# Performance work log

Measured on AMD Instinct MI355X. Metric: run time of the kernel, lower is better.

## Reference

```python
import jax, jax.numpy as jnp
import numpy as np

B, N, S, K, NDIM, HID = 2, 8192, 1024, 32, 3, 256


def _sincos_embed(pos, dim):
    # pos: (..., ndim) continuous coordinates -> (..., dim) sincos embedding
    ndim = pos.shape[-1]
    emb_dim_per_dim = dim // ndim
    half = emb_dim_per_dim // 2
    freq = jnp.exp(jnp.arange(half, dtype=pos.dtype) * (-np.log(10000.0) / (half - 1)))
    embs = []
    for i in range(ndim):
        e = pos[..., i:i + 1] * freq  # (..., half)
        embs.append(jnp.concatenate([jnp.sin(e), jnp.cos(e)], axis=-1))
    x = jnp.concatenate(embs, axis=-1)  # (..., ndim*2*half)
    pad = dim - x.shape[-1]
    if pad > 0:
        x = jnp.pad(x, [(0, 0)] * (x.ndim - 1) + [(0, pad)])
    return x


def setup_inputs() -> dict:
    key = jax.random.key(0)
    ks = jax.random.split(key, 8)
    input_pos = jax.random.normal(ks[0], (B, N, NDIM), dtype=jnp.float32)
    supernode_idxs = jax.random.randint(ks[1], (S,), 0, N)
    # lecun_normal-style init (stddev = 1/sqrt(fan_in)), zero bias (torch/flax Dense default bias=0)
    w_in = jax.random.normal(ks[2], (NDIM, HID), dtype=jnp.float32) / np.sqrt(NDIM)
    b_in = jnp.zeros((HID,), jnp.float32)
    w1 = jax.random.normal(ks[3], (HID, HID), dtype=jnp.float32) / np.sqrt(HID)
    b1 = jnp.zeros((HID,), jnp.float32)
    w2 = jax.random.normal(ks[4], (HID, HID), dtype=jnp.float32) / np.sqrt(HID)
    b2 = jnp.zeros((HID,), jnp.float32)
    return {"input_pos": input_pos, "supernode_idxs": supernode_idxs,
            "w_in": w_in, "b_in": b_in, "w1": w1, "b1": b1, "w2": w2, "b2": b2}


def reference(input_pos, supernode_idxs, w_in, b_in, w1, b1, w2, b2):
    def knn(x):  # x: (N, ndim)
        # Euclidean distance from each supernode to every point: (S, N).
        # Same values as rows of the full NxN cdist the original materializes.
        d = jnp.sqrt(jnp.sum((x[supernode_idxs][:, None, :] - x[None, :, :]) ** 2, axis=-1))
        nbr = jnp.argsort(d, axis=1)[:, :K]  # (S, K)
        return x[nbr]  # (S, K, ndim)

    coords = jax.vmap(knn)(input_pos)  # (B, S, K, ndim)
    proj = coords @ w_in + b_in                         # (B, S, K, HID)
    pe = _sincos_embed(coords, HID)                     # (B, S, K, HID)
    h = proj + pe
    h = jax.nn.gelu(h @ w1 + b1) @ w2 + b2              # message MLP
    return jnp.mean(h, axis=-2)                         # (B, S, HID)
```

## Files before the change

### kernel.cpp

```cpp
#include <hip/hip_runtime.h>
#include <hip/hip_bf16.h>
#include <math.h>

#define BB   2
#define NN   8192
#define SS   1024
#define KK   32
#define HID  256
#define NTH  256
#define PPT  64
#define SENT 0xFFFFFFFFFFFFFFFFULL
#define LDB  264
#define WFE  65536

typedef unsigned long long u64;
typedef unsigned int       u32;
typedef short bf16x8 __attribute__((ext_vector_type(8)));
typedef float f32x4  __attribute__((ext_vector_type(4)));

#define CSW(SI) { const u64 mn = x < (SI) ? x : (SI); const u64 mx = x < (SI) ? (SI) : x; (SI) = mn; x = mx; }
#define INS(KV) { u64 x = (KV); CSW(s0) CSW(s1) CSW(s2) CSW(s3) }

__device__ __forceinline__ float tanh_fast(float y) {
    const float e = __expf(2.0f * y);
    const float r = __builtin_amdgcn_rcpf(e + 1.0f);
    return fmaf(-2.0f, r, 1.0f);
}

__device__ __forceinline__ short bf_bits(float f) {
    const __hip_bfloat16 h = __float2bfloat16(f);
    short s;
    __builtin_memcpy(&s, &h, 2);
    return s;
}

__device__ __forceinline__ int mbcnt64(u64 m) {
    return (int)__builtin_amdgcn_mbcnt_hi((u32)(m >> 32),
           __builtin_amdgcn_mbcnt_lo((u32)m, 0u));
}

__global__ void prep_w(const float* __restrict__ w1, const float* __restrict__ w2,
                       __hip_bfloat16* __restrict__ wf) {
    const int idx = blockIdx.x * 256 + threadIdx.x;
    const int j   = idx & 7;
    const int l   = (idx >> 3) & 63;
    const int ntg = (idx >> 9) & 15;
    const int ks  = (idx >> 13) & 7;
    const int mat = idx >> 16;
    const int k = ks * 32 + (l >> 4) * 8 + j;
    const int n = ntg * 16 + (l & 15);
    const float v = (mat ? w2 : w1)[k * HID + n];
    const __hip_bfloat16 hi = __float2bfloat16(v);
    const float res = v - __bfloat162float(hi);
    const size_t s0 = (size_t)mat * 131072 + ((size_t)((ks*16 + ntg)*2) * 64 + l) * 8 + j;
    wf[s0]       = hi;
    wf[s0 + 512] = __float2bfloat16(res);
}

__global__ __launch_bounds__(NTH, 4)
void snp_kernel(const float* __restrict__ pos,
                const int*   __restrict__ snidx,
                const float* __restrict__ w_in,
                const float* __restrict__ b_in,
                const float* __restrict__ b1,
                const float* __restrict__ b2,
                const __hip_bfloat16* __restrict__ wf,
                float*       __restrict__ out)
{
    const int tk0  = blockIdx.x * 2;
    const int b    = tk0 / SS;
    const int s0i  = tk0 - b * SS;
    const int t    = threadIdx.x;
    const int lane = t & 63;
    const int wv   = t >> 6;
    const int tok  = t >> 7;
    const int pl   = t & 127;

    __shared__ __align__(16) short h0b[2 * KK][LDB];
    __shared__ u64   wl[4 * KK];
    __shared__ int   nbr[2 * KK];
    __shared__ __align__(16) float nbc[2 * 4 * KK];

    const float* posb = pos + (size_t)b * (NN * 3);
    const int  spA = snidx[s0i], spB = snidx[s0i + 1];
    const int  sp  = tok ? spB : spA;
    const float sx = posb[sp*3 + 0];
    const float sy = posb[sp*3 + 1];
    const float sz = posb[sp*3 + 2];

    u64 s0=SENT,s1=SENT,s2=SENT,s3=SENT;
#pragma unroll 4
    for (int c = 0; c < PPT; ++c) {
        const int i = c * 128 + pl;
        const float dx = __fsub_rn(sx, posb[i*3 + 0]);
        const float dy = __fsub_rn(sy, posb[i*3 + 1]);
        const float dz = __fsub_rn(sz, posb[i*3 + 2]);
        const float sq = __fadd_rn(__fadd_rn(__fmul_rn(dx,dx), __fmul_rn(dy,dy)),
                                   __fmul_rn(dz,dz));
        const u64 kv = ((u64)__float_as_uint(__fsqrt_rn(sq)) << 13) | (u32)i;
        INS(kv);
    }

    {
        u64 L = 0;
        for (int bit = 43; bit >= 13; --bit) {
            const u64 cand = L | (1ull << bit);
            const int cnt = __popcll(__ballot(s0 < cand)) + __popcll(__ballot(s1 < cand))
                          + __popcll(__ballot(s2 < cand)) + __popcll(__ballot(s3 < cand));
            if (cnt < 32) L = cand;
        }
        u64 TH = L + (1ull << 13);
        {
            const int cnt = __popcll(__ballot(s0 < TH)) + __popcll(__ballot(s1 < TH))
                          + __popcll(__ballot(s2 < TH)) + __popcll(__ballot(s3 < TH));
            if (cnt != 32) {
                for (int bit = 12; bit >= 0; --bit) {
                    const u64 cand = L | (1ull << bit);
                    const int c2 = __popcll(__ballot(s0 < cand)) + __popcll(__ballot(s1 < cand))
                                 + __popcll(__ballot(s2 < cand)) + __popcll(__ballot(s3 < cand));
                    if (c2 < 32) L = cand;
                }
                TH = L + 1;
            }
        }
        const bool b0 = s0 < TH, b1 = s1 < TH, b2 = s2 < TH, b3 = s3 < TH;
        const int csel = (int)b0 + (int)b1 + (int)b2 + (int)b3;

        if (__ballot(csel == 4) != 0ull) {
            int nv = 4;
#pragma unroll 1
            for (int it = 0; it < KK; ++it) {
                u64 m = s0;
#pragma unroll
                for (int off = 32; off > 0; off >>= 1) {
                    const u64 o = __shfl_xor(m, off, 64);
                    m = o < m ? o : m;
                }
                if (lane == 0) wl[wv*KK + it] = m;
                if (s0 == m) {
                    s0=s1; s1=s2; s2=s3; s3=SENT;
                    if (--nv == 0) {
                        const u64 last = m;
                        s0=s1=s2=s3=SENT;
#pragma unroll 4
                        for (int c = 0; c < PPT; ++c) {
                            const int i = c * 128 + pl;
                            const float dx = __fsub_rn(sx, posb[i*3 + 0]);
                            const float dy = __fsub_rn(sy, posb[i*3 + 1]);
                            const float dz = __fsub_rn(sz, posb[i*3 + 2]);
                            const float sq = __fadd_rn(__fadd_rn(__fmul_rn(dx,dx), __fmul_rn(dy,dy)),
                                                       __fmul_rn(dz,dz));
                            u64 kv = ((u64)__float_as_uint(__fsqrt_rn(sq)) << 13) | (u32)i;
                            kv = kv > last ? kv : SENT;
                            INS(kv);
                        }
                        nv = (int)(s0!=SENT)+(int)(s1!=SENT)+(int)(s2!=SENT)+(int)(s3!=SENT);
                    }
                }
            }
        } else {
            const u64 m0 = __ballot(b0), m1 = __ballot(b1),
                      m2 = __ballot(b2), m3 = __ballot(b3);
            const int pos2 = mbcnt64(m0) + mbcnt64(m1) + mbcnt64(m2) + mbcnt64(m3);
            u64* wwl = &wl[wv * KK];
            if (b0) wwl[pos2]     = s0;
            if (b1) wwl[pos2 + 1] = s1;
            if (b2) wwl[pos2 + 2] = s2;
            if (b3) wwl[pos2 + 3] = s3;
        }
    }
    __syncthreads();

    if (t < 128) {
        const u64 k0 = wl[wv * 64 + lane];
        u64 L = 0;
        for (int bit = 43; bit >= 13; --bit) {
            const u64 cand = L | (1ull << bit);
            if (__popcll(__ballot(k0 < cand)) < 32) L = cand;
        }
        u64 TH = L + (1ull << 13);
        if (__popcll(__ballot(k0 < TH)) != 32) {
            for (int bit = 12; bit >= 0; --bit) {
                const u64 cand = L | (1ull << bit);
                if (__popcll(__ballot(k0 < cand)) < 32) L = cand;
            }
            TH = L + 1;
        }
        const bool c0 = k0 < TH;
        const int p = mbcnt64(__ballot(c0));
        if (c0) nbr[wv * KK + p] = (int)(k0 & 8191u);
    }
    __syncthreads();

    if (t < 2 * KK * 3) {
        const int k = t / 3, d = t - 3 * k;
        nbc[k * 4 + d] = posb[(size_t)nbr[k] * 3 + d];
    }
    __syncthreads();

    {
        const int  c     = t;
        const int  dimi  = c / 84;
        const int  cc    = c - dimi * 84;
        const bool hasPe = c < 252;
        const bool isCos = cc >= 42;
        const int  f     = isCos ? cc - 42 : cc;
        const float fcoef = (float)(-9.210340371976184 / 41.0);
        const float freqv = expf((float)f * fcoef);
        const int  di    = hasPe ? dimi : 0;

        const float wi0 = w_in[0*HID + c];
        const float wi1 = w_in[1*HID + c];
        const float wi2 = w_in[2*HID + c];
        const float bi  = b_in[c];

#pragma unroll 4
        for (int k = 0; k < 2 * KK; ++k) {
            const float4 xv4 = *(const float4*)&nbc[k * 4];
            const float x0 = xv4.x, x1 = xv4.y, x2 = xv4.z;
            float v = fmaf(x2, wi2, fmaf(x1, wi1, fmaf(x0, wi0, bi)));
            if (hasPe) {
                const float xv  = (di == 0) ? x0 : ((di == 1) ? x1 : x2);
                const float ang = xv * freqv;
                v += isCos ? __cosf(ang) : __sinf(ang);
            }
            h0b[k][c] = bf_bits(v);
        }
    }
    __syncthreads();

    const int lr = lane & 15;
    const int lg = lane >> 4;
    const int nbase = wv * 64;

    const short* arow0 = &h0b[lr][lg * 8];
    const short* arow1 = &h0b[16 + lr][lg * 8];
    const short* arow2 = &h0b[32 + lr][lg * 8];
    const short* arow3 = &h0b[48 + lr][lg * 8];
    const __hip_bfloat16* wb1 = wf + (size_t)wv * 4096 + lane * 8;
    const __hip_bfloat16* wb2 = wb1 + 2 * WFE;

    f32x4 acc[4][4];

    {
#pragma unroll
        for (int nt = 0; nt < 4; ++nt) {
            const float bias = b1[nbase + nt*16 + lr];
            const f32x4 bv = {bias, bias, bias, bias};
            acc[0][nt] = bv; acc[1][nt] = bv; acc[2][nt] = bv; acc[3][nt] = bv;
        }
#pragma unroll 1
        for (int ks = 0; ks < 8; ++ks) {
            const bf16x8 af0 = *(const bf16x8*)(arow0 + ks * 32);
            const bf16x8 af1 = *(const bf16x8*)(arow1 + ks * 32);
            const bf16x8 af2 = *(const bf16x8*)(arow2 + ks * 32);
            const bf16x8 af3 = *(const bf16x8*)(arow3 + ks * 32);
            const __hip_bfloat16* p = wb1 + ks * 16384;
#pragma unroll
            for (int nt = 0; nt < 4; ++nt) {
                const bf16x8 bh = *(const bf16x8*)(p + nt * 1024);
                acc[0][nt] = __builtin_amdgcn_mfma_f32_16x16x32_bf16(af0, bh, acc[0][nt], 0,0,0);
                acc[1][nt] = __builtin_amdgcn_mfma_f32_16x16x32_bf16(af1, bh, acc[1][nt], 0,0,0);
                acc[2][nt] = __builtin_amdgcn_mfma_f32_16x16x32_bf16(af2, bh, acc[2][nt], 0,0,0);
                acc[3][nt] = __builtin_amdgcn_mfma_f32_16x16x32_bf16(af3, bh, acc[3][nt], 0,0,0);
                const bf16x8 bl = *(const bf16x8*)(p + nt * 1024 + 512);
                acc[0][nt] = __builtin_amdgcn_mfma_f32_16x16x32_bf16(af0, bl, acc[0][nt], 0,0,0);
                acc[1][nt] = __builtin_amdgcn_mfma_f32_16x16x32_bf16(af1, bl, acc[1][nt], 0,0,0);
                acc[2][nt] = __builtin_amdgcn_mfma_f32_16x16x32_bf16(af2, bl, acc[2][nt], 0,0,0);
                acc[3][nt] = __builtin_amdgcn_mfma_f32_16x16x32_bf16(af3, bl, acc[3][nt], 0,0,0);
            }
        }
    }
    __syncthreads();

    {
        const float kA = 0.7978845608028654f;
#pragma unroll
        for (int mt = 0; mt < 4; ++mt)
#pragma unroll
        for (int nt = 0; nt < 4; ++nt)
#pragma unroll
        for (int r = 0; r < 4; ++r) {
            const float x  = acc[mt][nt][r];
            const float x3 = x * x * x;
            const float tv = tanh_fast(kA * fmaf(0.044715f, x3, x));
            h0b[mt*16 + lg*4 + r][nbase + nt*16 + lr] = bf_bits(0.5f * x * (1.0f + tv));
        }
    }
    __syncthreads();

    {
        const f32x4 z = {0.f, 0.f, 0.f, 0.f};
#pragma unroll
        for (int nt = 0; nt < 4; ++nt) {
            acc[0][nt] = z; acc[1][nt] = z; acc[2][nt] = z; acc[3][nt] = z;
        }
#pragma unroll 1
        for (int ks = 0; ks < 8; ++ks) {
            const bf16x8 af0 = *(const bf16x8*)(arow0 + ks * 32);
            const bf16x8 af1 = *(const bf16x8*)(arow1 + ks * 32);
            const bf16x8 af2 = *(const bf16x8*)(arow2 + ks * 32);
            const bf16x8 af3 = *(const bf16x8*)(arow3 + ks * 32);
            const __hip_bfloat16* p = wb2 + ks * 16384;
#pragma unroll
            for (int nt = 0; nt < 4; ++nt) {
                const bf16x8 bh = *(const bf16x8*)(p + nt * 1024);
                acc[0][nt] = __builtin_amdgcn_mfma_f32_16x16x32_bf16(af0, bh, acc[0][nt], 0,0,0);
                acc[1][nt] = __builtin_amdgcn_mfma_f32_16x16x32_bf16(af1, bh, acc[1][nt], 0,0,0);
                acc[2][nt] = __builtin_amdgcn_mfma_f32_16x16x32_bf16(af2, bh, acc[2][nt], 0,0,0);
                acc[3][nt] = __builtin_amdgcn_mfma_f32_16x16x32_bf16(af3, bh, acc[3][nt], 0,0,0);
                const bf16x8 bl = *(const bf16x8*)(p + nt * 1024 + 512);
                acc[0][nt] = __builtin_amdgcn_mfma_f32_16x16x32_bf16(af0, bl, acc[0][nt], 0,0,0);
                acc[1][nt] = __builtin_amdgcn_mfma_f32_16x16x32_bf16(af1, bl, acc[1][nt], 0,0,0);
                acc[2][nt] = __builtin_amdgcn_mfma_f32_16x16x32_bf16(af2, bl, acc[2][nt], 0,0,0);
                acc[3][nt] = __builtin_amdgcn_mfma_f32_16x16x32_bf16(af3, bl, acc[3][nt], 0,0,0);
            }
        }
    }

#pragma unroll
    for (int nt = 0; nt < 4; ++nt) {
        float sumA = 0.0f, sumB = 0.0f;
#pragma unroll
        for (int r = 0; r < 4; ++r) {
            sumA += acc[0][nt][r] + acc[1][nt][r];
            sumB += acc[2][nt][r] + acc[3][nt][r];
        }
        sumA += __shfl_xor(sumA, 16, 64); sumA += __shfl_xor(sumA, 32, 64);
        sumB += __shfl_xor(sumB, 16, 64); sumB += __shfl_xor(sumB, 32, 64);
        if (lane < 16) {
            const int ch = nbase + nt*16 + lane;
            const float bb = b2[ch];
            out[(size_t)tk0 * HID + ch]       = fmaf(sumA, 1.0f / KK, bb);
            out[(size_t)(tk0 + 1) * HID + ch] = fmaf(sumB, 1.0f / KK, bb);
        }
    }
}

extern "C" void kernel_launch(void* const* d_in, const int* in_sizes, int n_in,
                              void* d_out, int out_size, void* d_ws, size_t ws_size,
                              hipStream_t stream) {
    const float* pos  = (const float*)d_in[0];
    const int*   sni  = (const int*)  d_in[1];
    const float* w_in = (const float*)d_in[2];
    const float* b_in = (const float*)d_in[3];
    const float* w1   = (const float*)d_in[4];
    const float* b1   = (const float*)d_in[5];
    const float* w2   = (const float*)d_in[6];
    const float* b2   = (const float*)d_in[7];
    float* out = (float*)d_out;
    __hip_bfloat16* wf = (__hip_bfloat16*)d_ws;
    (void)ws_size; (void)in_sizes; (void)n_in; (void)out_size;

    hipLaunchKernelGGL(prep_w, dim3(2 * WFE / 256), dim3(256), 0, stream, w1, w2, wf);
    hipLaunchKernelGGL(snp_kernel, dim3(BB * SS / 2), dim3(NTH), 0, stream,
                       pos, sni, w_in, b_in, b1, b2, wf, out);
}
```

Before: 86.40 us.

## Split fused kernel into separate kNN and MLP kernels with global neighbor buffer

The single fused kernel is split in two. A kNN kernel uses one block per supernode with all 256 threads scanning points, launch bounds allow 8 blocks per CU, and it writes neighbor indices to a global workspace buffer. A separate MLP kernel reads those indices and runs the MFMA message MLP. This separates the register and LDS needs of the selection and GEMM phases so each can reach higher occupancy. In exchange it adds a kernel launch and a global round trip for the neighbor indices.

Result: slower. 90.76 us (+5.1%).

```diff
diff --git a/kernel.cpp b/kernel.cpp
--- a/kernel.cpp
+++ b/kernel.cpp
@@ -7,8 +7,6 @@
 #define SS   1024
 #define KK   32
 #define HID  256
-#define NTH  256
-#define PPT  64
 #define SENT 0xFFFFFFFFFFFFFFFFULL
 #define LDB  264
 #define WFE  65536
@@ -57,41 +55,30 @@
     wf[s0 + 512] = __float2bfloat16(res);
 }
 
-__global__ __launch_bounds__(NTH, 4)
-void snp_kernel(const float* __restrict__ pos,
+__global__ __launch_bounds__(256, 8)
+void knn_kernel(const float* __restrict__ pos,
                 const int*   __restrict__ snidx,
-                const float* __restrict__ w_in,
-                const float* __restrict__ b_in,
-                const float* __restrict__ b1,
-                const float* __restrict__ b2,
-                const __hip_bfloat16* __restrict__ wf,
-                float*       __restrict__ out)
+                int*         __restrict__ nbr_g)
 {
-    const int tk0  = blockIdx.x * 2;
-    const int b    = tk0 / SS;
-    const int s0i  = tk0 - b * SS;
+    const int bs   = blockIdx.x;
+    const int b    = bs / SS;
+    const int s    = bs - b * SS;
     const int t    = threadIdx.x;
     const int lane = t & 63;
     const int wv   = t >> 6;
-    const int tok  = t >> 7;
-    const int pl   = t & 127;
-
-    __shared__ __align__(16) short h0b[2 * KK][LDB];
-    __shared__ u64   wl[4 * KK];
-    __shared__ int   nbr[2 * KK];
-    __shared__ __align__(16) float nbc[2 * 4 * KK];
+
+    __shared__ u64 wl[4 * KK];
 
     const float* posb = pos + (size_t)b * (NN * 3);
-    const int  spA = snidx[s0i], spB = snidx[s0i + 1];
-    const int  sp  = tok ? spB : spA;
+    const int   sp = snidx[s];
     const float sx = posb[sp*3 + 0];
     const float sy = posb[sp*3 + 1];
     const float sz = posb[sp*3 + 2];
 
     u64 s0=SENT,s1=SENT,s2=SENT,s3=SENT;
 #pragma unroll 4
-    for (int c = 0; c < PPT; ++c) {
-        const int i = c * 128 + pl;
+    for (int c = 0; c < 32; ++c) {
+        const int i = c * 256 + t;
         const float dx = __fsub_rn(sx, posb[i*3 + 0]);
         const float dy = __fsub_rn(sy, posb[i*3 + 1]);
         const float dz = __fsub_rn(sz, posb[i*3 + 2]);
@@ -143,8 +130,8 @@
                         const u64 last = m;
                         s0=s1=s2=s3=SENT;
 #pragma unroll 4
-                        for (int c = 0; c < PPT; ++c) {
-                            const int i = c * 128 + pl;
+                        for (int c = 0; c < 32; ++c) {
+                            const int i = c * 256 + t;
                             const float dx = __fsub_rn(sx, posb[i*3 + 0]);
                             const float dy = __fsub_rn(sy, posb[i*3 + 1]);
                             const float dz = __fsub_rn(sz, posb[i*3 + 2]);
@@ -171,30 +158,57 @@
     }
     __syncthreads();
 
-    if (t < 128) {
-        const u64 k0 = wl[wv * 64 + lane];
+    if (t < 64) {
+        const u64 k0 = wl[lane], k1 = wl[64 + lane];
         u64 L = 0;
         for (int bit = 43; bit >= 13; --bit) {
             const u64 cand = L | (1ull << bit);
-            if (__popcll(__ballot(k0 < cand)) < 32) L = cand;
+            const int cnt = __popcll(__ballot(k0 < cand)) + __popcll(__ballot(k1 < cand));
+            if (cnt < 32) L = cand;
         }
         u64 TH = L + (1ull << 13);
-        if (__popcll(__ballot(k0 < TH)) != 32) {
-            for (int bit = 12; bit >= 0; --bit) {
-                const u64 cand = L | (1ull << bit);
-                if (__popcll(__ballot(k0 < cand)) < 32) L = cand;
-            }
-            TH = L + 1;
-        }
-        const bool c0 = k0 < TH;
-        const int p = mbcnt64(__ballot(c0));
-        if (c0) nbr[wv * KK + p] = (int)(k0 & 8191u);
-    }
-    __syncthreads();
+        {
+            const int cnt = __popcll(__ballot(k0 < TH)) + __popcll(__ballot(k1 < TH));
+            if (cnt != 32) {
+                for (int bit = 12; bit >= 0; --bit) {
+                    const u64 cand = L | (1ull << bit);
+                    const int c2 = __popcll(__ballot(k0 < cand)) + __popcll(__ballot(k1 < cand));
+                    if (c2 < 32) L = cand;
+                }
+                TH = L + 1;
+            }
+        }
+        const bool c0 = k0 < TH, c1 = k1 < TH;
+        const int p = mbcnt64(__ballot(c0)) + mbcnt64(__ballot(c1));
+        if (c0) nbr_g[(size_t)bs * KK + p]           = (int)(k0 & 8191u);
+        if (c1) nbr_g[(size_t)bs * KK + p + (int)c0] = (int)(k1 & 8191u);
+    }
+}
+
+__global__ __launch_bounds__(256, 4)
+void mlp_kernel(const float* __restrict__ pos,
+                const int*   __restrict__ nbr_g,
+                const float* __restrict__ w_in,
+                const float* __restrict__ b_in,
+                const float* __restrict__ b1,
+                const float* __restrict__ b2,
+                const __hip_bfloat16* __restrict__ wf,
+                float*       __restrict__ out)
+{
+    const int tk0  = blockIdx.x * 2;
+    const int b    = tk0 / SS;
+    const int t    = threadIdx.x;
+    const int lane = t & 63;
+    const int wv   = t >> 6;
+
+    __shared__ __align__(16) short h0b[2 * KK][LDB];
+    __shared__ __align__(16) float nbc[2 * 4 * KK];
+
+    const float* posb = pos + (size_t)b * (NN * 3);
 
     if (t < 2 * KK * 3) {
         const int k = t / 3, d = t - 3 * k;
-        nbc[k * 4 + d] = posb[(size_t)nbr[k] * 3 + d];
+        nbc[k * 4 + d] = posb[(size_t)nbr_g[(size_t)tk0 * KK + k] * 3 + d];
     }
     __syncthreads();
 
@@ -329,7 +343,7 @@
         sumA += __shfl_xor(sumA, 16, 64); sumA += __shfl_xor(sumA, 32, 64);
         sumB += __shfl_xor(sumB, 16, 64); sumB += __shfl_xor(sumB, 32, 64);
         if (lane < 16) {
-            const int ch = nbase + nt*16 + lane;
+            const int ch = wv * 64 + nt*16 + lane;
             const float bb = b2[ch];
             out[(size_t)tk0 * HID + ch]       = fmaf(sumA, 1.0f / KK, bb);
             out[(size_t)(tk0 + 1) * HID + ch] = fmaf(sumB, 1.0f / KK, bb);
@@ -350,9 +364,11 @@
     const float* b2   = (const float*)d_in[7];
     float* out = (float*)d_out;
     __hip_bfloat16* wf = (__hip_bfloat16*)d_ws;
+    int* nbr_g = (int*)((char*)d_ws + 4 * WFE * 2);
     (void)ws_size; (void)in_sizes; (void)n_in; (void)out_size;
 
     hipLaunchKernelGGL(prep_w, dim3(2 * WFE / 256), dim3(256), 0, stream, w1, w2, wf);
-    hipLaunchKernelGGL(snp_kernel, dim3(BB * SS / 2), dim3(NTH), 0, stream,
-                       pos, sni, w_in, b_in, b1, b2, wf, out);
-}
+    hipLaunchKernelGGL(knn_kernel, dim3(BB * SS), dim3(256), 0, stream, pos, sni, nbr_g);
+    hipLaunchKernelGGL(mlp_kernel, dim3(BB * SS / 2), dim3(256), 0, stream,
+                       pos, nbr_g, w_in, b_in, b1, b2, wf, out);
+}
```
